# Kernel optimization log

Measured on AMD Instinct MI355X. Metric: run time of the kernel, lower is better.

## Reference

```python
import jax, jax.numpy as jnp
import numpy as np
import math

DIM_EMB = 1024
DIM_QK = 1024
DIM_V = 1024
NORM_FACT = 1.0 / math.sqrt(DIM_EMB)

def setup_inputs() -> dict:
    key = jax.random.key(0)
    k0, k1, k2, k3 = jax.random.split(key, 4)
    x = jax.random.normal(k0, (4, 4096, DIM_EMB), dtype=jnp.float32)
    # nn.Linear weights are [out_features, in_features]; y = x @ W.T
    s = 1.0 / math.sqrt(DIM_EMB)
    Wq = jax.random.uniform(k1, (DIM_QK, DIM_EMB), jnp.float32, -s, s)
    Wk = jax.random.uniform(k2, (DIM_QK, DIM_EMB), jnp.float32, -s, s)
    Wv = jax.random.uniform(k3, (DIM_V, DIM_EMB), jnp.float32, -s, s)
    return {"x": x, "Wq": Wq, "Wk": Wk, "Wv": Wv}

def reference(x, Wq, Wk, Wv):
    # q,k,v: [b, n, d]
    q = jnp.einsum('bne,de->bnd', x, Wq)
    k = jnp.einsum('bne,de->bnd', x, Wk)
    v = jnp.einsum('bne,de->bnd', x, Wv)
    logits = jnp.einsum('bnd,bmd->bnm', q, k)  # [b, n, n]
    # Faithful to source: softmax over last dim FIRST, then scale by 1/sqrt(dim_embedding)
    score = jax.nn.softmax(logits, axis=-1) * NORM_FACT
    att = jnp.einsum('bnm,bmv->bnv', score, v)
    return att
```

## Files before the change

### kernel.cpp

```cpp
#include <hip/hip_runtime.h>
#include <hip/hip_bf16.h>

typedef _Float16 f16;
typedef _Float16 f16x4 __attribute__((ext_vector_type(4)));
typedef _Float16 f16x8 __attribute__((ext_vector_type(8)));
typedef float f32x4 __attribute__((ext_vector_type(4)));

__device__ __forceinline__ void gload16(const void* g, void* l) {
    __builtin_amdgcn_global_load_lds(
        (const __attribute__((address_space(1))) void*)g,
        (__attribute__((address_space(3))) void*)l, 16, 0, 0);
}

#define FENCE asm volatile("" ::: "memory")
#define BARRIER do { FENCE; __builtin_amdgcn_s_barrier(); FENCE; } while (0)

#define PHASE_MFMA(QI, QJ)                                                    \
    __builtin_amdgcn_s_setprio(1);                                            \
    _Pragma("unroll")                                                         \
    for (int ks = 0; ks < 2; ++ks)                                            \
      _Pragma("unroll")                                                       \
      for (int i = 0; i < 4; ++i)                                             \
        _Pragma("unroll")                                                     \
        for (int j = 0; j < 2; ++j)                                           \
          acc[(QI)*4 + i][(QJ)*2 + j] = __builtin_amdgcn_mfma_f32_16x16x32_f16( \
              a[i][ks], b[j][ks], acc[(QI)*4 + i][(QJ)*2 + j], 0, 0, 0);      \
    __builtin_amdgcn_s_setprio(0);

template<bool F16OUT>
__global__ __launch_bounds__(512) void gemm_bt8(
    const f16* __restrict__ A, const f16* __restrict__ B, void* __restrict__ Cv,
    int K, int lda, int ldb, int ldc, float scale, int nbn)
{
    __shared__ f16 sA[2][256 * 64];
    __shared__ f16 sB[2][256 * 64];
    const int tid = threadIdx.x, lane = tid & 63, wid = tid >> 6;
    const int wr = wid >> 2, wc = wid & 3;

    const int cpx = gridDim.x >> 3;
    const int wg = (blockIdx.x & 7) * cpx + (blockIdx.x >> 3);
    const int bm = (wg / nbn) << 8, bn = (wg % nbn) << 8;

    const int rr8 = lane >> 3;
    const int cs  = ((lane & 7) ^ rr8) << 3;
    const int ldsr = wid << 3;

    auto stageA = [&](int kt, int c, int h) {
        const size_t g0 = (size_t)(bm + (h << 7) + ldsr + rr8) * lda + kt + cs;
        gload16(A + g0,                      &sA[c][((h << 7) + ldsr) << 6]);
        gload16(A + g0 + ((size_t)lda << 6), &sA[c][((h << 7) + 64 + ldsr) << 6]);
    };
    auto stageB = [&](int kt, int c, int h) {
        const size_t g0 = (size_t)(bn + (h << 7) + ldsr + rr8) * ldb + kt + cs;
        gload16(B + g0,                      &sB[c][((h << 7) + ldsr) << 6]);
        gload16(B + g0 + ((size_t)ldb << 6), &sB[c][((h << 7) + 64 + ldsr) << 6]);
    };

    f32x4 acc[8][4] = {};
    f16x8 a[4][2], b[2][2];

    auto loadA = [&](int c, int qi) {
#pragma unroll
        for (int i = 0; i < 4; ++i) {
            const int ra = wr * 128 + (qi * 4 + i) * 16 + (lane & 15);
            const int swz = (ra & 7) << 3;
#pragma unroll
            for (int ks = 0; ks < 2; ++ks) {
                const int kk = ks * 32 + (lane >> 4) * 8;
                a[i][ks] = *(const f16x8*)(&sA[c][(ra << 6) + (kk ^ swz)]);
            }
        }
    };
    auto loadB = [&](int c, int qj) {
#pragma unroll
        for (int j = 0; j < 2; ++j) {
            const int rb = wc * 64 + (qj * 2 + j) * 16 + (lane & 15);
            const int swz = (rb & 7) << 3;
#pragma unroll
            for (int ks = 0; ks < 2; ++ks) {
                const int kk = ks * 32 + (lane >> 4) * 8;
                b[j][ks] = *(const f16x8*)(&sB[c][(rb << 6) + (kk ^ swz)]);
            }
        }
    };

    stageA(0, 0, 0); stageA(0, 0, 1); stageB(0, 0, 0); stageB(0, 0, 1);
    asm volatile("s_waitcnt vmcnt(0)" ::: "memory");
    BARRIER;

    const int NT = K >> 6;
    for (int g = 0; g < NT; ++g) {
        const int c = g & 1, cn = c ^ 1;
        const int kn = (g + 1) << 6;
        const bool more = (g + 1) < NT;
        loadA(c, 0); loadB(c, 0);
        if (more) { stageA(kn, cn, 0); stageA(kn, cn, 1); }
        BARRIER; PHASE_MFMA(0, 0); BARRIER;
        loadB(c, 1);
        if (more) { stageB(kn, cn, 0); stageB(kn, cn, 1); }
        BARRIER; PHASE_MFMA(0, 1); BARRIER;
        loadA(c, 1); loadB(c, 0);
        BARRIER; PHASE_MFMA(1, 0); BARRIER;
        loadB(c, 1);
        asm volatile("s_waitcnt vmcnt(0)" ::: "memory");
        BARRIER; PHASE_MFMA(1, 1); BARRIER;
    }
#pragma unroll
    for (int i = 0; i < 8; ++i)
#pragma unroll
        for (int j = 0; j < 4; ++j)
#pragma unroll
            for (int r = 0; r < 4; ++r) {
                const int row = bm + wr * 128 + i * 16 + ((lane >> 4) << 2) + r;
                const int col = bn + wc * 64 + j * 16 + (lane & 15);
                if constexpr (F16OUT)
                    ((f16*)Cv)[(size_t)row * ldc + col] = (f16)(acc[i][j][r] * scale);
                else
                    ((float*)Cv)[(size_t)row * ldc + col] = acc[i][j][r] * scale;
            }
}

template<bool F16IN, bool F16OUT, bool PIPE>
__global__ __launch_bounds__(256) void gemm_bt(
    const void* __restrict__ Av, const void* __restrict__ Bv, void* __restrict__ Cv,
    int K, int lda, int ldb, int ldc, float scale)
{
    constexpr int NB = PIPE ? 2 : 1;
    __shared__ f16 sA[NB][128 * 64];
    __shared__ f16 sB[NB][128 * 64];
    const int tid = threadIdx.x, lane = tid & 63, wid = tid >> 6;
    const int wr = wid >> 1, wc = wid & 1;
    const int bm = blockIdx.x * 128, bn = blockIdx.y * 128;

    f32x4 acc[4][4] = {};

    auto stage16 = [&](int kt, int bsel) {
        const f16* A = (const f16*)Av;
        const f16* B = (const f16*)Bv;
        const int rsub = lane >> 3;
        const int csw = ((lane & 7) ^ rsub) << 3;
#pragma unroll
        for (int i = 0; i < 4; ++i) {
            const int rb = (wid * 4 + i) * 8;
            gload16(A + (size_t)(bm + rb + rsub) * lda + kt + csw, &sA[bsel][rb * 64]);
            gload16(B + (size_t)(bn + rb + rsub) * ldb + kt + csw, &sB[bsel][rb * 64]);
        }
    };

    auto compute = [&](int bsel) {
#pragma unroll
        for (int ks = 0; ks < 2; ++ks) {
            const int kk = ks * 32 + (lane >> 4) * 8;
            f16x8 a[4], b[4];
#pragma unroll
            for (int i = 0; i < 4; ++i) {
                const int ra = wr * 64 + i * 16 + (lane & 15);
                a[i] = *(const f16x8*)(&sA[bsel][(ra << 6) + (kk ^ ((ra & 7) << 3))]);
                const int rb2 = wc * 64 + i * 16 + (lane & 15);
                b[i] = *(const f16x8*)(&sB[bsel][(rb2 << 6) + (kk ^ ((rb2 & 7) << 3))]);
            }
#pragma unroll
            for (int i = 0; i < 4; ++i)
#pragma unroll
                for (int j = 0; j < 4; ++j)
                    acc[i][j] = __builtin_amdgcn_mfma_f32_16x16x32_f16(a[i], b[j], acc[i][j], 0, 0, 0);
        }
    };

    if constexpr (PIPE) {
        static_assert(F16IN, "PIPE requires f16 inputs");
        stage16(0, 0);
        asm volatile("s_waitcnt vmcnt(0)" ::: "memory");
        __syncthreads();
        const int NT2 = K >> 6;
        for (int t = 0; t < NT2; ++t) {
            if (t + 1 < NT2) stage16((t + 1) << 6, (t + 1) & 1);
            compute(t & 1);
            asm volatile("s_waitcnt vmcnt(0)" ::: "memory");
            __builtin_amdgcn_s_barrier();
        }
    } else {
        for (int kt = 0; kt < K; kt += 64) {
            __syncthreads();
            if constexpr (F16IN) {
                stage16(kt, 0);
            } else {
                const float* A = (const float*)Av;
                const float* B = (const float*)Bv;
                const int r0 = tid >> 4;
                const int c4 = (tid & 15) << 2;
#pragma unroll
                for (int p = 0; p < 8; ++p) {
                    const int row = (p << 4) + r0;
                    const float4 av = *(const float4*)(A + (size_t)(bm + row) * lda + kt + c4);
                    const float4 bv = *(const float4*)(B + (size_t)(bn + row) * ldb + kt + c4);
                    const int sc = c4 ^ ((row & 7) << 3);
                    f16x4 ah = { (f16)av.x, (f16)av.y, (f16)av.z, (f16)av.w };
                    f16x4 bh = { (f16)bv.x, (f16)bv.y, (f16)bv.z, (f16)bv.w };
                    *(f16x4*)(&sA[0][(row << 6) + sc]) = ah;
                    *(f16x4*)(&sB[0][(row << 6) + sc]) = bh;
                }
            }
            __syncthreads();
            compute(0);
        }
    }
#pragma unroll
    for (int i = 0; i < 4; ++i)
#pragma unroll
        for (int j = 0; j < 4; ++j)
#pragma unroll
            for (int r = 0; r < 4; ++r) {
                const int row = bm + wr * 64 + i * 16 + (lane >> 4) * 4 + r;
                const int col = bn + wc * 64 + j * 16 + (lane & 15);
                if constexpr (F16OUT)
                    ((f16*)Cv)[(size_t)row * ldc + col] = (f16)acc[i][j][r];
                else
                    ((float*)Cv)[(size_t)row * ldc + col] = acc[i][j][r] * scale;
            }
}

__global__ __launch_bounds__(256) void cvt_f16(
    const float* __restrict__ s, f16* __restrict__ d, int n8)
{
    int i = blockIdx.x * 256 + threadIdx.x;
    const int stride = gridDim.x * 256;
    for (; i < n8; i += stride) {
        const float4 a = ((const float4*)s)[i * 2];
        const float4 b = ((const float4*)s)[i * 2 + 1];
        f16x8 o = { (f16)a.x, (f16)a.y, (f16)a.z, (f16)a.w,
                    (f16)b.x, (f16)b.y, (f16)b.z, (f16)b.w };
        ((f16x8*)d)[i] = o;
    }
}

__global__ __launch_bounds__(256) void softmax_inplace(float* S)
{
    const int lane = threadIdx.x & 63, wid = threadIdx.x >> 6;
    const int row = blockIdx.x * 4 + wid;
    float* src = S + (size_t)row * 4096;
    float4 v[16];
#pragma unroll
    for (int u = 0; u < 16; ++u)
        v[u] = ((const float4*)src)[u * 64 + lane];
    float m = -1e30f;
#pragma unroll
    for (int u = 0; u < 16; ++u)
        m = fmaxf(m, fmaxf(fmaxf(v[u].x, v[u].y), fmaxf(v[u].z, v[u].w)));
#pragma unroll
    for (int msk = 1; msk <= 32; msk <<= 1) m = fmaxf(m, __shfl_xor(m, msk));
    float s = 0.f;
#pragma unroll
    for (int u = 0; u < 16; ++u) {
        v[u].x = __expf(v[u].x - m); v[u].y = __expf(v[u].y - m);
        v[u].z = __expf(v[u].z - m); v[u].w = __expf(v[u].w - m);
        s += (v[u].x + v[u].y) + (v[u].z + v[u].w);
    }
#pragma unroll
    for (int msk = 1; msk <= 32; msk <<= 1) s += __shfl_xor(s, msk);
    const float inv = 1.0f / s;
    f16* dst = (f16*)S + (size_t)row * 8192;
#pragma unroll
    for (int u = 0; u < 16; ++u) {
        f16x4 p = { (f16)(v[u].x * inv), (f16)(v[u].y * inv),
                    (f16)(v[u].z * inv), (f16)(v[u].w * inv) };
        *(f16x4*)(dst + u * 256 + lane * 4) = p;
    }
}

extern "C" void kernel_launch(void* const* d_in, const int* in_sizes, int n_in,
                              void* d_out, int out_size, void* d_ws, size_t ws_size,
                              hipStream_t stream) {
    const float* x  = (const float*)d_in[0];
    const float* Wq = (const float*)d_in[1];
    const float* Wk = (const float*)d_in[2];
    const float* Wv = (const float*)d_in[3];
    float* out = (float*)d_out;

    f16*   qk  = (f16*)d_out;
    f16*   xh  = (f16*)d_ws;
    f16*   wqh = xh + 16384LL * 1024;
    f16*   wkh = wqh + 1024LL * 1024;
    float* Sf  = (float*)d_ws;
    f16*   Sh  = (f16*)d_ws;

    cvt_f16<<<1024, 256, 0, stream>>>(x,  xh,  16384 * 1024 / 8);
    cvt_f16<<<512,  256, 0, stream>>>(Wq, wqh, 1024 * 1024 / 8);
    cvt_f16<<<512,  256, 0, stream>>>(Wk, wkh, 1024 * 1024 / 8);

    gemm_bt8<true><<<256, 512, 0, stream>>>(xh, wqh, qk,        1024, 1024, 1024, 2048, 1.f, 4);
    gemm_bt8<true><<<256, 512, 0, stream>>>(xh, wkh, qk + 1024, 1024, 1024, 1024, 2048, 1.f, 4);

    for (int b = 0; b < 4; ++b) {
        const size_t tb = (size_t)b * 4096;
        gemm_bt8<false><<<256, 512, 0, stream>>>(
            qk + tb * 2048, qk + tb * 2048 + 1024, Sf,
            1024, 2048, 2048, 4096, 1.f, 16);
        softmax_inplace<<<1024, 256, 0, stream>>>(Sf);
        gemm_bt<false, true, false><<<dim3(8, 32), 256, 0, stream>>>(
            Wv, x + tb * 1024, Sh + 3072LL * 8192 + 4096,
            1024, 1024, 1024, 8192, 1.f);
        gemm_bt<true, false, true><<<dim3(32, 8), 256, 0, stream>>>(
            Sh, Sh + 3072LL * 8192 + 4096, out + tb * 1024,
            4096, 8192, 8192, 1024, 1.f / 32.f);
    }
}
```

Before: 649.9 us.

## Split-K PV GEMM with atomics and pre-convert V inputs to f16

Replaces the PV product kernel with a new 512-thread, double-buffered kernel using global-to-LDS loads, split along K into two halves that accumulate into a zeroed output with atomicAdd. The V projection now reads pre-converted f16 copies of x and Wv, held in the output buffer, through the f16 staging path instead of converting fp32 inline. The fp32-staging branch of the generic GEMM is removed. This aims to raise occupancy and overlap memory traffic with compute in the PV stage, at the cost of extra conversion and zeroing launches plus atomic traffic.

After: 654.6 us. No clear change (+0.7%).

```diff
diff --git a/kernel.cpp b/kernel.cpp
--- a/kernel.cpp
+++ b/kernel.cpp
@@ -168,7 +168,6 @@
     };
 
     if constexpr (PIPE) {
-        static_assert(F16IN, "PIPE requires f16 inputs");
         stage16(0, 0);
         asm volatile("s_waitcnt vmcnt(0)" ::: "memory");
         __syncthreads();
@@ -182,25 +181,7 @@
     } else {
         for (int kt = 0; kt < K; kt += 64) {
             __syncthreads();
-            if constexpr (F16IN) {
-                stage16(kt, 0);
-            } else {
-                const float* A = (const float*)Av;
-                const float* B = (const float*)Bv;
-                const int r0 = tid >> 4;
-                const int c4 = (tid & 15) << 2;
-#pragma unroll
-                for (int p = 0; p < 8; ++p) {
-                    const int row = (p << 4) + r0;
-                    const float4 av = *(const float4*)(A + (size_t)(bm + row) * lda + kt + c4);
-                    const float4 bv = *(const float4*)(B + (size_t)(bn + row) * ldb + kt + c4);
-                    const int sc = c4 ^ ((row & 7) << 3);
-                    f16x4 ah = { (f16)av.x, (f16)av.y, (f16)av.z, (f16)av.w };
-                    f16x4 bh = { (f16)bv.x, (f16)bv.y, (f16)bv.z, (f16)bv.w };
-                    *(f16x4*)(&sA[0][(row << 6) + sc]) = ah;
-                    *(f16x4*)(&sB[0][(row << 6) + sc]) = bh;
-                }
-            }
+            stage16(kt, 0);
             __syncthreads();
             compute(0);
         }
@@ -217,6 +198,77 @@
                     ((f16*)Cv)[(size_t)row * ldc + col] = (f16)acc[i][j][r];
                 else
                     ((float*)Cv)[(size_t)row * ldc + col] = acc[i][j][r] * scale;
+            }
+}
+
+__global__ __launch_bounds__(512) void gemm_pv(
+    const f16* __restrict__ A, const f16* __restrict__ B, float* __restrict__ C,
+    int lda, int ldb, int ldc, float scale)
+{
+    __shared__ f16 sA[2][128 * 64];
+    __shared__ f16 sB[2][128 * 64];
+    const int tid = threadIdx.x, lane = tid & 63, wid = tid >> 6;
+    const int wr = wid >> 2, wc = wid & 3;
+    const int bm = blockIdx.x * 128, bn = blockIdx.y * 128;
+    const int kbase = blockIdx.z * 2048;
+
+    const int rr8 = lane >> 3;
+    const int cs  = ((lane & 7) ^ rr8) << 3;
+    const int ldsr = wid << 3;
+
+    auto stage = [&](int kt, int c) {
+        const size_t a0 = (size_t)(bm + ldsr + rr8) * lda + kbase + kt + cs;
+        gload16(A + a0,                      &sA[c][ldsr << 6]);
+        gload16(A + a0 + ((size_t)lda << 6), &sA[c][(64 + ldsr) << 6]);
+        const size_t b0 = (size_t)(bn + ldsr + rr8) * ldb + kbase + kt + cs;
+        gload16(B + b0,                      &sB[c][ldsr << 6]);
+        gload16(B + b0 + ((size_t)ldb << 6), &sB[c][(64 + ldsr) << 6]);
+    };
+
+    f32x4 acc[4][2] = {};
+
+    stage(0, 0);
+    asm volatile("s_waitcnt vmcnt(0)" ::: "memory");
+    BARRIER;
+
+    for (int t = 0; t < 32; ++t) {
+        if (t + 1 < 32) stage((t + 1) << 6, (t + 1) & 1);
+        const f16* pa = sA[t & 1];
+        const f16* pb = sB[t & 1];
+        __builtin_amdgcn_s_setprio(1);
+#pragma unroll
+        for (int ks = 0; ks < 2; ++ks) {
+            const int kk = ks * 32 + (lane >> 4) * 8;
+            f16x8 a[4], b[2];
+#pragma unroll
+            for (int i = 0; i < 4; ++i) {
+                const int ra = wr * 64 + i * 16 + (lane & 15);
+                a[i] = *(const f16x8*)(pa + (ra << 6) + (kk ^ ((ra & 7) << 3)));
+            }
+#pragma unroll
+            for (int j = 0; j < 2; ++j) {
+                const int rb = wc * 32 + j * 16 + (lane & 15);
+                b[j] = *(const f16x8*)(pb + (rb << 6) + (kk ^ ((rb & 7) << 3)));
+            }
+#pragma unroll
+            for (int i = 0; i < 4; ++i)
+#pragma unroll
+                for (int j = 0; j < 2; ++j)
+                    acc[i][j] = __builtin_amdgcn_mfma_f32_16x16x32_f16(a[i], b[j], acc[i][j], 0, 0, 0);
+        }
+        __builtin_amdgcn_s_setprio(0);
+        asm volatile("s_waitcnt vmcnt(0)" ::: "memory");
+        BARRIER;
+    }
+#pragma unroll
+    for (int i = 0; i < 4; ++i)
+#pragma unroll
+        for (int j = 0; j < 2; ++j)
+#pragma unroll
+            for (int r = 0; r < 4; ++r) {
+                const int row = bm + wr * 64 + i * 16 + ((lane >> 4) << 2) + r;
+                const int col = bn + wc * 32 + j * 16 + (lane & 15);
+                atomicAdd(&C[(size_t)row * ldc + col], acc[i][j][r] * scale);
             }
 }
 
@@ -234,6 +286,14 @@
     }
 }
 
+__global__ __launch_bounds__(256) void zerof(float* __restrict__ p, int n4)
+{
+    int i = blockIdx.x * 256 + threadIdx.x;
+    const int stride = gridDim.x * 256;
+    const float4 z = {0.f, 0.f, 0.f, 0.f};
+    for (; i < n4; i += stride) ((float4*)p)[i] = z;
+}
+
 __global__ __launch_bounds__(256) void softmax_inplace(float* S)
 {
     const int lane = threadIdx.x & 63, wid = threadIdx.x >> 6;
@@ -283,6 +343,7 @@
     f16*   wkh = wqh + 1024LL * 1024;
     float* Sf  = (float*)d_ws;
     f16*   Sh  = (f16*)d_ws;
+    f16*   vTp = Sh + 3072LL * 8192 + 4096;
 
     cvt_f16<<<1024, 256, 0, stream>>>(x,  xh,  16384 * 1024 / 8);
     cvt_f16<<<512,  256, 0, stream>>>(Wq, wqh, 1024 * 1024 / 8);
@@ -293,15 +354,18 @@
 
     for (int b = 0; b < 4; ++b) {
         const size_t tb = (size_t)b * 4096;
+        f16* xhb = (f16*)(out + tb * 1024);
+        f16* wvh = xhb + 4096LL * 1024;
         gemm_bt8<false><<<256, 512, 0, stream>>>(
             qk + tb * 2048, qk + tb * 2048 + 1024, Sf,
             1024, 2048, 2048, 4096, 1.f, 16);
         softmax_inplace<<<1024, 256, 0, stream>>>(Sf);
-        gemm_bt<false, true, false><<<dim3(8, 32), 256, 0, stream>>>(
-            Wv, x + tb * 1024, Sh + 3072LL * 8192 + 4096,
-            1024, 1024, 1024, 8192, 1.f);
-        gemm_bt<true, false, true><<<dim3(32, 8), 256, 0, stream>>>(
-            Sh, Sh + 3072LL * 8192 + 4096, out + tb * 1024,
-            4096, 8192, 8192, 1024, 1.f / 32.f);
-    }
-}
+        cvt_f16<<<1024, 256, 0, stream>>>(x + tb * 1024, xhb, 4096 * 1024 / 8);
+        cvt_f16<<<512,  256, 0, stream>>>(Wv, wvh, 1024 * 1024 / 8);
+        gemm_bt<true, true, true><<<dim3(8, 32), 256, 0, stream>>>(
+            wvh, xhb, vTp, 1024, 1024, 1024, 8192, 1.f);
+        zerof<<<2048, 256, 0, stream>>>(out + tb * 1024, 4096 * 1024 / 4);
+        gemm_pv<<<dim3(32, 8, 2), 512, 0, stream>>>(
+            Sh, vTp, out + tb * 1024, 8192, 8192, 1024, 1.f / 32.f);
+    }
+}
```
